# Performance work log

Hardware: AMD Instinct MI355X
Metric: run time of the kernel (lower is better)

Reference implementation:

```python
import jax, jax.numpy as jnp
import numpy as np

B, S, D, H = 2, 2048, 768, 12
DK = D // H
NEG = -1000000000.0


def setup_inputs() -> dict:
    key = jax.random.key(0)
    ks = jax.random.split(key, 12)
    inp = {
        "query": jax.random.normal(ks[0], (B, S, D), jnp.float32),
        "key": jax.random.normal(ks[1], (B, S, D), jnp.float32),
        "value": jax.random.normal(ks[2], (B, S, D), jnp.float32),
        "mask": jax.random.randint(ks[3], (B, 1, 1, S), 0, 2, jnp.int32),
    }
    sc = 1.0 / np.sqrt(D)
    inp["Wq"] = jax.random.normal(ks[4], (D, D), jnp.float32) * sc
    inp["bq"] = jnp.zeros((D,), jnp.float32)
    inp["Wk"] = jax.random.normal(ks[5], (D, D), jnp.float32) * sc
    inp["bk"] = jnp.zeros((D,), jnp.float32)
    inp["Wv"] = jax.random.normal(ks[6], (D, D), jnp.float32) * sc
    inp["bv"] = jnp.zeros((D,), jnp.float32)
    inp["Wo"] = jax.random.normal(ks[7], (D, D), jnp.float32) * sc
    inp["bo"] = jnp.zeros((D,), jnp.float32)
    return inp


def reference(query, key, value, mask, Wq, bq, Wk, bk, Wv, bv, Wo, bo):
    b = query.shape[0]
    # QKV projections -> [B, H, S, DK]
    def proj(x, W, bias):
        y = jnp.einsum('bsd,de->bse', x, W.T) + bias
        return y.reshape(b, -1, H, DK).transpose(0, 2, 1, 3)
    q = proj(query, Wq, bq)
    k = proj(key, Wk, bk)
    v = proj(value, Wv, bv)
    # scores: [B, H, S, S]
    scores = jnp.einsum('bhqd,bhkd->bhqk', q, k) / jnp.sqrt(jnp.float32(DK))
    scores = jnp.where(mask == 0, jnp.float32(NEG), scores)
    p = jax.nn.softmax(scores, axis=-1)
    x = jnp.einsum('bhqk,bhkd->bhqd', p, v)  # [B, H, S, DK]
    x = x.transpose(0, 2, 1, 3).reshape(b, -1, H * DK)
    return jnp.einsum('bsd,de->bse', x, Wo.T) + bo
```

## Files before the change

### kernel.cpp

```cpp
#include <hip/hip_runtime.h>

typedef unsigned short u16;
typedef __attribute__((ext_vector_type(8))) __bf16 bf16x8;
typedef __attribute__((ext_vector_type(8))) short s16x8;
typedef __attribute__((ext_vector_type(8))) unsigned short u16x8;
typedef __attribute__((ext_vector_type(4))) float f32x4;
typedef __attribute__((ext_vector_type(4))) unsigned short u16x4;
typedef __attribute__((ext_vector_type(4))) float fl4;
typedef __attribute__((ext_vector_type(4))) int i32x4;

#define MFMA(a, b, c) __builtin_amdgcn_mfma_f32_16x16x32_bf16((a), (b), (c), 0, 0, 0)
#define QSC 0.18033688011112042f

__device__ __forceinline__ u16 f2bf(float f) {
  union { float f; unsigned u; } v; v.f = f;
  unsigned u = v.u;
  return (u16)((u + 0x7fffu + ((u >> 16) & 1u)) >> 16);
}

__device__ __forceinline__ float bf2f(u16 u) {
  union { unsigned u; float f; } v; v.u = ((unsigned)u) << 16;
  return v.f;
}

__device__ __forceinline__ void gll16(const u16* g, u16* l) {
  typedef __attribute__((address_space(1))) unsigned int gu32;
  typedef __attribute__((address_space(3))) unsigned int lu32;
  __builtin_amdgcn_global_load_lds((gu32*)g, (lu32*)l, 16, 0, 0);
}


__global__ __launch_bounds__(256) void k_convert_x(
    const float* __restrict__ q, const float* __restrict__ k,
    const float* __restrict__ v, u16* __restrict__ xb) {
  const int NG = 4096 * 768 / 4;
  const int n = 3 * NG;
  for (int i = blockIdx.x * 256 + threadIdx.x; i < n; i += gridDim.x * 256) {
    int seg = i / NG;
    int j = (i - seg * NG) * 4;
    const float* s = (seg == 0) ? q : ((seg == 1) ? k : v);
    fl4 f = *(const fl4*)(s + j);
    u16x4 o;
    o[0] = f2bf(f[0]); o[1] = f2bf(f[1]); o[2] = f2bf(f[2]); o[3] = f2bf(f[3]);
    *(u16x4*)(xb + seg * (4096 * 768) + j) = o;
  }
}

__global__ __launch_bounds__(256) void k_convert_w(
    const float* __restrict__ Wq, const float* __restrict__ Wk,
    const float* __restrict__ Wv, const float* __restrict__ Wo,
    u16* __restrict__ wqkv, u16* __restrict__ wob) {
  const int n = 3072 * 192;
  for (int i = blockIdx.x * 256 + threadIdx.x; i < n; i += gridDim.x * 256) {
    int row = i / 192;
    int col = (i - row * 192) * 4;
    const float* src; u16* dst; float sc = 1.0f;
    if (row < 768)       { src = Wq + row * 768;          dst = wqkv + row * 768; sc = QSC; }
    else if (row < 1536) { src = Wk + (row - 768) * 768;  dst = wqkv + row * 768; }
    else if (row < 2304) { src = Wv + (row - 1536) * 768; dst = wqkv + row * 768; }
    else                 { src = Wo + (row - 2304) * 768; dst = wob + (row - 2304) * 768; }
    fl4 f = *(const fl4*)(src + col);
    u16x4 o;
    o[0] = f2bf(f[0] * sc); o[1] = f2bf(f[1] * sc);
    o[2] = f2bf(f[2] * sc); o[3] = f2bf(f[3] * sc);
    *(u16x4*)(dst + col) = o;
  }
}


__global__ __launch_bounds__(256) void k_gemm_qkv(
    const u16* __restrict__ xb, const u16* __restrict__ wqkv,
    const float* __restrict__ bq, const float* __restrict__ bk_,
    const float* __restrict__ bv_,
    u16* __restrict__ Qb, u16* __restrict__ Kb, u16* __restrict__ Vtb) {
  __shared__ __align__(16) u16 As[128 * 32];
  __shared__ __align__(16) u16 Bs[128 * 32];
  const int tid = threadIdx.x;
  const int row0 = blockIdx.x * 128, col0 = blockIdx.y * 128;
  const int seg = col0 / 768;
  const u16* A = xb + (size_t)seg * (4096 * 768);
  const int w = tid >> 6, lane = tid & 63, lr = lane & 15, kg = lane >> 4;
  const int wr = (w >> 1) * 64, wc = (w & 1) * 64;

  const int c0 = tid, c1 = tid + 256;
  const int r0c = c0 >> 2, p0 = c0 & 3, g0 = p0 ^ ((r0c >> 1) & 3);
  const int r1c = c1 >> 2, p1 = c1 & 3, g1 = p1 ^ ((r1c >> 1) & 3);

  f32x4 acc[4][4];
  f32x4 zero = {0.f, 0.f, 0.f, 0.f};
#pragma unroll
  for (int i = 0; i < 4; i++)
#pragma unroll
    for (int j = 0; j < 4; j++) acc[i][j] = zero;

  int aoff[4], boff[4];
#pragma unroll
  for (int mi = 0; mi < 4; mi++) {
    int r = wr + mi * 16 + lr;
    aoff[mi] = r * 32 + (kg ^ ((r >> 1) & 3)) * 8;
  }
#pragma unroll
  for (int ni = 0; ni < 4; ni++) {
    int r = wc + ni * 16 + lr;
    boff[ni] = r * 32 + (kg ^ ((r >> 1) & 3)) * 8;
  }

  for (int kt = 0; kt < 24; kt++) {
    const int k0 = kt * 32;
    gll16(A + (row0 + r0c) * 768 + k0 + g0 * 8, As + c0 * 8);
    gll16(A + (row0 + r1c) * 768 + k0 + g1 * 8, As + c1 * 8);
    gll16(wqkv + (col0 + r0c) * 768 + k0 + g0 * 8, Bs + c0 * 8);
    gll16(wqkv + (col0 + r1c) * 768 + k0 + g1 * 8, Bs + c1 * 8);
    __syncthreads();
    bf16x8 af[4], bfr[4];
#pragma unroll
    for (int mi = 0; mi < 4; mi++) af[mi] = *(const bf16x8*)(As + aoff[mi]);
#pragma unroll
    for (int ni = 0; ni < 4; ni++) bfr[ni] = *(const bf16x8*)(Bs + boff[ni]);
#pragma unroll
    for (int mi = 0; mi < 4; mi++)
#pragma unroll
      for (int ni = 0; ni < 4; ni++)
        acc[mi][ni] = MFMA(af[mi], bfr[ni], acc[mi][ni]);
    __syncthreads();
  }

  const float* bias = (seg == 0) ? bq : ((seg == 1) ? bk_ : bv_);
  const float bsc = (seg == 0) ? QSC : 1.0f;
  const int ncol0 = col0 - seg * 768;
#pragma unroll
  for (int ni = 0; ni < 4; ni++) {
    const int n = ncol0 + wc + ni * 16 + lr;
    const float bval = bias[n] * bsc;
    const int hh = n >> 6, dk = n & 63;
#pragma unroll
    for (int mi = 0; mi < 4; mi++)
#pragma unroll
      for (int j = 0; j < 4; j++) {
        const int m = row0 + wr + mi * 16 + kg * 4 + j;
        const int bb = m >> 11, ss = m & 2047;
        const u16 val = f2bf(acc[mi][ni][j] + bval);
        if (seg == 0)
          Qb[((size_t)((bb * 12 + hh) * 2048 + ss)) * 64 + dk] = val;
        else if (seg == 1)
          Kb[((size_t)((bb * 12 + hh) * 2048 + ss)) * 64 + dk] = val;
        else
          Vtb[((size_t)((bb * 12 + hh) * 64 + dk)) * 2048 + ss] = val;
      }
  }
}


__global__ __launch_bounds__(256) void k_attn(
    const u16* __restrict__ Qb, const u16* __restrict__ Kb,
    const u16* __restrict__ Vtb, const int* __restrict__ mask,
    u16* __restrict__ o_part, float* __restrict__ l_part) {
  __shared__ __align__(16) u16 Ks[2][64 * 64];
  __shared__ __align__(16) u16 Vs[2][64 * 64];
  __shared__ __align__(16) u16 Ps[4][32 * 64];
  __shared__ __align__(16) int mlds[1024];
  const int bh = blockIdx.y, b = bh / 12;
  const int half = blockIdx.z;
  const int kvb = half << 10;
  const int tid = threadIdx.x, w = tid >> 6, lane = tid & 63;
  const int lr = lane & 15, g = lane >> 4;
  const int q0 = blockIdx.x * 128 + w * 32;
  const u16* Qh = Qb + (size_t)bh * (2048 * 64);
  const u16* Kh = Kb + (size_t)bh * (2048 * 64);
  const u16* Vh = Vtb + (size_t)bh * (64 * 2048);
  const int* mb = mask + b * 2048;
  u16* Pw = Ps[w];

  *(i32x4*)(mlds + tid * 4) = *(const i32x4*)(mb + kvb + tid * 4);

  bf16x8 aq[2][2];
#pragma unroll
  for (int mi = 0; mi < 2; mi++)
#pragma unroll
    for (int ks = 0; ks < 2; ks++)
      aq[mi][ks] = *(const bf16x8*)(Qh + (q0 + mi * 16 + lr) * 64 + ks * 32 + g * 8);

  f32x4 zero = {0.f, 0.f, 0.f, 0.f};
  f32x4 o[2][4];
#pragma unroll
  for (int mi = 0; mi < 2; mi++)
#pragma unroll
    for (int di = 0; di < 4; di++) o[mi][di] = zero;
  f32x4 o_l[2];
  o_l[0] = zero; o_l[1] = zero;

  s16x8 ov = {0x3F80, 0x3F80, 0x3F80, 0x3F80, 0x3F80, 0x3F80, 0x3F80, 0x3F80};
  bf16x8 ones = __builtin_bit_cast(bf16x8, ov);

  const int c0 = tid, c1 = tid + 256;
  const int sr0 = c0 >> 3, sg0 = (c0 & 7) ^ (sr0 & 7);
  const int sr1 = c1 >> 3, sg1 = (c1 & 7) ^ (sr1 & 7);
  const u16* kA0 = Kh + (size_t)kvb * 64 + sr0 * 64 + sg0 * 8;
  const u16* kA1 = Kh + (size_t)kvb * 64 + sr1 * 64 + sg1 * 8;
  const u16* vA0 = Vh + sr0 * 2048 + kvb + sg0 * 8;
  const u16* vA1 = Vh + sr1 * 2048 + kvb + sg1 * 8;

#define STAGE(u) { u16* kd = Ks[(u)&1]; u16* vd = Vs[(u)&1];           \
    gll16(kA0 + (u) * 4096, kd + c0 * 8);                              \
    gll16(kA1 + (u) * 4096, kd + c1 * 8);                              \
    gll16(vA0 + (u) * 64,  vd + c0 * 8);                               \
    gll16(vA1 + (u) * 64,  vd + c1 * 8); }

  STAGE(0);
  __syncthreads();

  for (int t = 0; t < 16; t++) {
    if (t < 15) STAGE(t + 1);
    const u16* Kc = Ks[t & 1];
    const u16* Vc = Vs[t & 1];

    f32x4 s[2][4];
#pragma unroll
    for (int ni = 0; ni < 4; ni++) {
      const int row = ni * 16 + lr;
      bf16x8 b0 = *(const bf16x8*)(Kc + row * 64 + ((g ^ (row & 7)) << 3));
      bf16x8 b1 = *(const bf16x8*)(Kc + row * 64 + (((4 + g) ^ (row & 7)) << 3));
#pragma unroll
      for (int mi = 0; mi < 2; mi++) {
        f32x4 z = zero;
        z = MFMA(aq[mi][0], b0, z);
        z = MFMA(aq[mi][1], b1, z);
        s[mi][ni] = z;
      }
    }
    int mk[4];
#pragma unroll
    for (int ni = 0; ni < 4; ni++) mk[ni] = mlds[t * 64 + ni * 16 + lr];
#pragma unroll
    for (int mi = 0; mi < 2; mi++)
#pragma unroll
      for (int ni = 0; ni < 4; ni++)
#pragma unroll
        for (int j = 0; j < 4; j++)
          s[mi][ni][j] = mk[ni] ? s[mi][ni][j] : -1e9f;

#pragma unroll
    for (int mi = 0; mi < 2; mi++)
#pragma unroll
      for (int ni = 0; ni < 4; ni++)
#pragma unroll
        for (int j = 0; j < 4; j++) {
          const float p = __builtin_amdgcn_exp2f(s[mi][ni][j]);
          const int prow = mi * 16 + g * 4 + j;
          const int byt = prow * 128 + ((ni * 32 + lr * 2) ^ ((prow & 7) << 4));
          Pw[byt >> 1] = f2bf(p);
        }

#pragma unroll
    for (int ks2 = 0; ks2 < 2; ks2++) {
      bf16x8 ap[2];
#pragma unroll
      for (int mi = 0; mi < 2; mi++) {
        const int prow = mi * 16 + lr;
        const int byt = prow * 128 + ((ks2 * 64 + g * 16) ^ ((prow & 7) << 4));
        ap[mi] = *(const bf16x8*)(Pw + (byt >> 1));
      }
#pragma unroll
      for (int di = 0; di < 4; di++) {
        const int vrow = di * 16 + lr;
        bf16x8 bv = *(const bf16x8*)(Vc + vrow * 64 + (((ks2 * 4 + g) ^ (vrow & 7)) << 3));
#pragma unroll
        for (int mi = 0; mi < 2; mi++)
          o[mi][di] = MFMA(ap[mi], bv, o[mi][di]);
      }
#pragma unroll
      for (int mi = 0; mi < 2; mi++)
        o_l[mi] = MFMA(ap[mi], ones, o_l[mi]);
    }

    if (t < 15) __syncthreads();
  }
#undef STAGE

  u16* opw = o_part + (size_t)(half * 24 + bh) * (2048 * 64);
  float* lpw = l_part + (size_t)(half * 24 + bh) * 2048;
#pragma unroll
  for (int mi = 0; mi < 2; mi++) {
#pragma unroll
    for (int di = 0; di < 4; di++)
#pragma unroll
      for (int j = 0; j < 4; j++) {
        const int row = q0 + mi * 16 + g * 4 + j;
        opw[(size_t)row * 64 + di * 16 + lr] = f2bf(o[mi][di][j]);
      }
    if (lr == 0) {
#pragma unroll
      for (int j = 0; j < 4; j++)
        lpw[q0 + mi * 16 + g * 4 + j] = o_l[mi][j];
    }
  }
}


__global__ __launch_bounds__(256) void k_combine(
    const u16* __restrict__ o_part, const float* __restrict__ l_part,
    u16* __restrict__ attn) {
  const int idx = blockIdx.x * 256 + threadIdx.x;
  const int row = idx >> 3;
  const int c8 = (idx & 7) << 3;
  const size_t HALF_O = (size_t)24 * 2048 * 64;
  u16x8 a0 = *(const u16x8*)(o_part + (size_t)row * 64 + c8);
  u16x8 a1 = *(const u16x8*)(o_part + HALF_O + (size_t)row * 64 + c8);
  const float l = l_part[row] + l_part[24 * 2048 + row];
  const float rcp = 1.0f / l;
  u16x8 r;
#pragma unroll
  for (int j = 0; j < 8; j++)
    r[j] = f2bf((bf2f(a0[j]) + bf2f(a1[j])) * rcp);
  const int bh = row >> 11, s = row & 2047;
  const int b = bh / 12, h = bh - b * 12;
  *(u16x8*)(attn + (size_t)(b * 2048 + s) * 768 + h * 64 + c8) = r;
}


__global__ __launch_bounds__(256) void k_gemm_out(
    const u16* __restrict__ attn, const u16* __restrict__ wob,
    const float* __restrict__ bo, float* __restrict__ out) {
  __shared__ __align__(16) u16 As[128 * 32];
  __shared__ __align__(16) u16 Bs[128 * 32];
  const int tid = threadIdx.x;
  const int row0 = blockIdx.x * 128, col0 = blockIdx.y * 128;
  const int w = tid >> 6, lane = tid & 63, lr = lane & 15, kg = lane >> 4;
  const int wr = (w >> 1) * 64, wc = (w & 1) * 64;

  const int c0 = tid, c1 = tid + 256;
  const int r0c = c0 >> 2, p0 = c0 & 3, g0 = p0 ^ ((r0c >> 1) & 3);
  const int r1c = c1 >> 2, p1 = c1 & 3, g1 = p1 ^ ((r1c >> 1) & 3);

  f32x4 acc[4][4];
  f32x4 zero = {0.f, 0.f, 0.f, 0.f};
#pragma unroll
  for (int i = 0; i < 4; i++)
#pragma unroll
    for (int j = 0; j < 4; j++) acc[i][j] = zero;

  int aoff[4], boff[4];
#pragma unroll
  for (int mi = 0; mi < 4; mi++) {
    int r = wr + mi * 16 + lr;
    aoff[mi] = r * 32 + (kg ^ ((r >> 1) & 3)) * 8;
  }
#pragma unroll
  for (int ni = 0; ni < 4; ni++) {
    int r = wc + ni * 16 + lr;
    boff[ni] = r * 32 + (kg ^ ((r >> 1) & 3)) * 8;
  }

  for (int kt = 0; kt < 24; kt++) {
    const int k0 = kt * 32;
    gll16(attn + (row0 + r0c) * 768 + k0 + g0 * 8, As + c0 * 8);
    gll16(attn + (row0 + r1c) * 768 + k0 + g1 * 8, As + c1 * 8);
    gll16(wob + (col0 + r0c) * 768 + k0 + g0 * 8, Bs + c0 * 8);
    gll16(wob + (col0 + r1c) * 768 + k0 + g1 * 8, Bs + c1 * 8);
    __syncthreads();
    bf16x8 af[4], bfr[4];
#pragma unroll
    for (int mi = 0; mi < 4; mi++) af[mi] = *(const bf16x8*)(As + aoff[mi]);
#pragma unroll
    for (int ni = 0; ni < 4; ni++) bfr[ni] = *(const bf16x8*)(Bs + boff[ni]);
#pragma unroll
    for (int mi = 0; mi < 4; mi++)
#pragma unroll
      for (int ni = 0; ni < 4; ni++)
        acc[mi][ni] = MFMA(af[mi], bfr[ni], acc[mi][ni]);
    __syncthreads();
  }

#pragma unroll
  for (int ni = 0; ni < 4; ni++) {
    const int n = col0 + wc + ni * 16 + lr;
    const float bval = bo[n];
#pragma unroll
    for (int mi = 0; mi < 4; mi++)
#pragma unroll
      for (int j = 0; j < 4; j++) {
        const int m = row0 + wr + mi * 16 + kg * 4 + j;
        out[(size_t)m * 768 + n] = acc[mi][ni][j] + bval;
      }
  }
}


extern "C" void kernel_launch(void* const* d_in, const int* in_sizes, int n_in,
                              void* d_out, int out_size, void* d_ws, size_t ws_size,
                              hipStream_t stream) {
  const float* q = (const float*)d_in[0];
  const float* k = (const float*)d_in[1];
  const float* v = (const float*)d_in[2];
  const int* mask = (const int*)d_in[3];
  const float* Wq = (const float*)d_in[4];
  const float* bq = (const float*)d_in[5];
  const float* Wk = (const float*)d_in[6];
  const float* bk = (const float*)d_in[7];
  const float* Wv = (const float*)d_in[8];
  const float* bv = (const float*)d_in[9];
  const float* Wo = (const float*)d_in[10];
  const float* bo = (const float*)d_in[11];
  float* out = (float*)d_out;

  u16* xb = (u16*)d_ws;
  u16* wqkv = xb + (size_t)3 * 4096 * 768;
  u16* wob = wqkv + (size_t)2304 * 768;
  u16* Qb = wob + (size_t)768 * 768;
  u16* Kb = Qb + (size_t)4096 * 768;
  u16* Vtb = Kb + (size_t)4096 * 768;
  u16* attn = Vtb + (size_t)4096 * 768;

  u16* o_part = xb;
  float* l_part = (float*)(xb + (size_t)2 * 24 * 2048 * 64);

  k_convert_x<<<dim3(4608), dim3(256), 0, stream>>>(q, k, v, xb);
  k_convert_w<<<dim3(2304), dim3(256), 0, stream>>>(Wq, Wk, Wv, Wo, wqkv, wob);
  k_gemm_qkv<<<dim3(32, 18), dim3(256), 0, stream>>>(xb, wqkv, bq, bk, bv, Qb, Kb, Vtb);
  k_attn<<<dim3(16, 24, 2), dim3(256), 0, stream>>>(Qb, Kb, Vtb, mask, o_part, l_part);
  k_combine<<<dim3(1536), dim3(256), 0, stream>>>(o_part, l_part, attn);
  k_gemm_out<<<dim3(32, 6), dim3(256), 0, stream>>>(attn, wob, bo, out);
}
```

Measured before the change: 123.7 us.

## Fuse fp32-to-bf16 input conversion into QKV GEMM and double-buffer GEMM tiles

Removes the separate activation conversion kernel: the QKV GEMM now loads fp32 inputs into registers, converts them to bf16 and writes them to LDS. Both GEMMs gain double-buffered LDS tiles so the next k-tile's loads are issued before the current tile's MFMAs. The f2bf helper switches to the compiler's native bf16 cast. This trades one kernel launch and a round trip of 3x4096x768 bf16 data for heavier register traffic in the QKV GEMM, with each A tile now read as fp32 once per column-block, roughly six times per segment.

```diff
diff --git a/kernel.cpp b/kernel.cpp
--- a/kernel.cpp
+++ b/kernel.cpp
@@ -13,9 +13,8 @@
 #define QSC 0.18033688011112042f
 
 __device__ __forceinline__ u16 f2bf(float f) {
-  union { float f; unsigned u; } v; v.f = f;
-  unsigned u = v.u;
-  return (u16)((u + 0x7fffu + ((u >> 16) & 1u)) >> 16);
+  __bf16 h = (__bf16)f;
+  return __builtin_bit_cast(unsigned short, h);
 }
 
 __device__ __forceinline__ float bf2f(u16 u) {
@@ -29,22 +28,6 @@
   __builtin_amdgcn_global_load_lds((gu32*)g, (lu32*)l, 16, 0, 0);
 }
 
-
-__global__ __launch_bounds__(256) void k_convert_x(
-    const float* __restrict__ q, const float* __restrict__ k,
-    const float* __restrict__ v, u16* __restrict__ xb) {
-  const int NG = 4096 * 768 / 4;
-  const int n = 3 * NG;
-  for (int i = blockIdx.x * 256 + threadIdx.x; i < n; i += gridDim.x * 256) {
-    int seg = i / NG;
-    int j = (i - seg * NG) * 4;
-    const float* s = (seg == 0) ? q : ((seg == 1) ? k : v);
-    fl4 f = *(const fl4*)(s + j);
-    u16x4 o;
-    o[0] = f2bf(f[0]); o[1] = f2bf(f[1]); o[2] = f2bf(f[2]); o[3] = f2bf(f[3]);
-    *(u16x4*)(xb + seg * (4096 * 768) + j) = o;
-  }
-}
 
 __global__ __launch_bounds__(256) void k_convert_w(
     const float* __restrict__ Wq, const float* __restrict__ Wk,
@@ -69,22 +52,27 @@
 
 
 __global__ __launch_bounds__(256) void k_gemm_qkv(
-    const u16* __restrict__ xb, const u16* __restrict__ wqkv,
+    const float* __restrict__ xq, const float* __restrict__ xk,
+    const float* __restrict__ xv, const u16* __restrict__ wqkv,
     const float* __restrict__ bq, const float* __restrict__ bk_,
     const float* __restrict__ bv_,
     u16* __restrict__ Qb, u16* __restrict__ Kb, u16* __restrict__ Vtb) {
-  __shared__ __align__(16) u16 As[128 * 32];
-  __shared__ __align__(16) u16 Bs[128 * 32];
+  __shared__ __align__(16) u16 Abuf[2][128 * 32];
+  __shared__ __align__(16) u16 Bbuf[2][128 * 32];
   const int tid = threadIdx.x;
   const int row0 = blockIdx.x * 128, col0 = blockIdx.y * 128;
   const int seg = col0 / 768;
-  const u16* A = xb + (size_t)seg * (4096 * 768);
+  const float* A32 = (seg == 0) ? xq : ((seg == 1) ? xk : xv);
   const int w = tid >> 6, lane = tid & 63, lr = lane & 15, kg = lane >> 4;
   const int wr = (w >> 1) * 64, wc = (w & 1) * 64;
 
   const int c0 = tid, c1 = tid + 256;
   const int r0c = c0 >> 2, p0 = c0 & 3, g0 = p0 ^ ((r0c >> 1) & 3);
   const int r1c = c1 >> 2, p1 = c1 & 3, g1 = p1 ^ ((r1c >> 1) & 3);
+  const float* aS0 = A32 + (size_t)(row0 + r0c) * 768 + g0 * 8;
+  const float* aS1 = A32 + (size_t)(row0 + r1c) * 768 + g1 * 8;
+  const u16* bS0 = wqkv + (size_t)(col0 + r0c) * 768 + g0 * 8;
+  const u16* bS1 = wqkv + (size_t)(col0 + r1c) * 768 + g1 * 8;
 
   f32x4 acc[4][4];
   f32x4 zero = {0.f, 0.f, 0.f, 0.f};
@@ -105,25 +93,47 @@
     boff[ni] = r * 32 + (kg ^ ((r >> 1) & 3)) * 8;
   }
 
+  fl4 ar[4];
+#define LOADA(kt) { ar[0] = *(const fl4*)(aS0 + (kt) * 32);       \
+                    ar[1] = *(const fl4*)(aS0 + (kt) * 32 + 4);   \
+                    ar[2] = *(const fl4*)(aS1 + (kt) * 32);       \
+                    ar[3] = *(const fl4*)(aS1 + (kt) * 32 + 4); }
+#define WRITEA(buf) { u16x8 t0, t1;                               \
+    t0[0]=f2bf(ar[0][0]); t0[1]=f2bf(ar[0][1]); t0[2]=f2bf(ar[0][2]); t0[3]=f2bf(ar[0][3]); \
+    t0[4]=f2bf(ar[1][0]); t0[5]=f2bf(ar[1][1]); t0[6]=f2bf(ar[1][2]); t0[7]=f2bf(ar[1][3]); \
+    t1[0]=f2bf(ar[2][0]); t1[1]=f2bf(ar[2][1]); t1[2]=f2bf(ar[2][2]); t1[3]=f2bf(ar[2][3]); \
+    t1[4]=f2bf(ar[3][0]); t1[5]=f2bf(ar[3][1]); t1[6]=f2bf(ar[3][2]); t1[7]=f2bf(ar[3][3]); \
+    *(u16x8*)((buf) + c0 * 8) = t0; *(u16x8*)((buf) + c1 * 8) = t1; }
+#define STAGEB(kt, buf) { gll16(bS0 + (kt) * 32, (buf) + c0 * 8); \
+                          gll16(bS1 + (kt) * 32, (buf) + c1 * 8); }
+
+  LOADA(0);
+  STAGEB(0, Bbuf[0]);
+  WRITEA(Abuf[0]);
+  __syncthreads();
+
   for (int kt = 0; kt < 24; kt++) {
-    const int k0 = kt * 32;
-    gll16(A + (row0 + r0c) * 768 + k0 + g0 * 8, As + c0 * 8);
-    gll16(A + (row0 + r1c) * 768 + k0 + g1 * 8, As + c1 * 8);
-    gll16(wqkv + (col0 + r0c) * 768 + k0 + g0 * 8, Bs + c0 * 8);
-    gll16(wqkv + (col0 + r1c) * 768 + k0 + g1 * 8, Bs + c1 * 8);
-    __syncthreads();
+    const int cur = kt & 1;
+    if (kt < 23) { LOADA(kt + 1); STAGEB(kt + 1, Bbuf[cur ^ 1]); }
     bf16x8 af[4], bfr[4];
 #pragma unroll
-    for (int mi = 0; mi < 4; mi++) af[mi] = *(const bf16x8*)(As + aoff[mi]);
-#pragma unroll
-    for (int ni = 0; ni < 4; ni++) bfr[ni] = *(const bf16x8*)(Bs + boff[ni]);
+    for (int mi = 0; mi < 4; mi++) af[mi] = *(const bf16x8*)(Abuf[cur] + aoff[mi]);
+#pragma unroll
+    for (int ni = 0; ni < 4; ni++) bfr[ni] = *(const bf16x8*)(Bbuf[cur] + boff[ni]);
 #pragma unroll
     for (int mi = 0; mi < 4; mi++)
 #pragma unroll
       for (int ni = 0; ni < 4; ni++)
         acc[mi][ni] = MFMA(af[mi], bfr[ni], acc[mi][ni]);
     __syncthreads();
-  }
+    if (kt < 23) {
+      WRITEA(Abuf[cur ^ 1]);
+      __syncthreads();
+    }
+  }
+#undef LOADA
+#undef WRITEA
+#undef STAGEB
 
   const float* bias = (seg == 0) ? bq : ((seg == 1) ? bk_ : bv_);
   const float bsc = (seg == 0) ? QSC : 1.0f;
@@ -321,8 +331,8 @@
 __global__ __launch_bounds__(256) void k_gemm_out(
     const u16* __restrict__ attn, const u16* __restrict__ wob,
     const float* __restrict__ bo, float* __restrict__ out) {
-  __shared__ __align__(16) u16 As[128 * 32];
-  __shared__ __align__(16) u16 Bs[128 * 32];
+  __shared__ __align__(16) u16 As[2][128 * 32];
+  __shared__ __align__(16) u16 Bs[2][128 * 32];
   const int tid = threadIdx.x;
   const int row0 = blockIdx.x * 128, col0 = blockIdx.y * 128;
   const int w = tid >> 6, lane = tid & 63, lr = lane & 15, kg = lane >> 4;
@@ -331,6 +341,10 @@
   const int c0 = tid, c1 = tid + 256;
   const int r0c = c0 >> 2, p0 = c0 & 3, g0 = p0 ^ ((r0c >> 1) & 3);
   const int r1c = c1 >> 2, p1 = c1 & 3, g1 = p1 ^ ((r1c >> 1) & 3);
+  const u16* aS0 = attn + (size_t)(row0 + r0c) * 768 + g0 * 8;
+  const u16* aS1 = attn + (size_t)(row0 + r1c) * 768 + g1 * 8;
+  const u16* bS0 = wob + (size_t)(col0 + r0c) * 768 + g0 * 8;
+  const u16* bS1 = wob + (size_t)(col0 + r1c) * 768 + g1 * 8;
 
   f32x4 acc[4][4];
   f32x4 zero = {0.f, 0.f, 0.f, 0.f};
@@ -351,25 +365,31 @@
     boff[ni] = r * 32 + (kg ^ ((r >> 1) & 3)) * 8;
   }
 
+#define STAGE(kt) { u16* ad = As[(kt)&1]; u16* bd = Bs[(kt)&1];   \
+    gll16(aS0 + (kt) * 32, ad + c0 * 8);                          \
+    gll16(aS1 + (kt) * 32, ad + c1 * 8);                          \
+    gll16(bS0 + (kt) * 32, bd + c0 * 8);                          \
+    gll16(bS1 + (kt) * 32, bd + c1 * 8); }
+
+  STAGE(0);
+  __syncthreads();
+
   for (int kt = 0; kt < 24; kt++) {
-    const int k0 = kt * 32;
-    gll16(attn + (row0 + r0c) * 768 + k0 + g0 * 8, As + c0 * 8);
-    gll16(attn + (row0 + r1c) * 768 + k0 + g1 * 8, As + c1 * 8);
-    gll16(wob + (col0 + r0c) * 768 + k0 + g0 * 8, Bs + c0 * 8);
-    gll16(wob + (col0 + r1c) * 768 + k0 + g1 * 8, Bs + c1 * 8);
-    __syncthreads();
+    const int cur = kt & 1;
+    if (kt < 23) STAGE(kt + 1);
     bf16x8 af[4], bfr[4];
 #pragma unroll
-    for (int mi = 0; mi < 4; mi++) af[mi] = *(const bf16x8*)(As + aoff[mi]);
-#pragma unroll
-    for (int ni = 0; ni < 4; ni++) bfr[ni] = *(const bf16x8*)(Bs + boff[ni]);
+    for (int mi = 0; mi < 4; mi++) af[mi] = *(const bf16x8*)(As[cur] + aoff[mi]);
+#pragma unroll
+    for (int ni = 0; ni < 4; ni++) bfr[ni] = *(const bf16x8*)(Bs[cur] + boff[ni]);
 #pragma unroll
     for (int mi = 0; mi < 4; mi++)
 #pragma unroll
       for (int ni = 0; ni < 4; ni++)
         acc[mi][ni] = MFMA(af[mi], bfr[ni], acc[mi][ni]);
-    __syncthreads();
-  }
+    if (kt < 23) __syncthreads();
+  }
+#undef STAGE
 
 #pragma unroll
   for (int ni = 0; ni < 4; ni++) {
@@ -403,20 +423,19 @@
   const float* bo = (const float*)d_in[11];
   float* out = (float*)d_out;
 
-  u16* xb = (u16*)d_ws;
-  u16* wqkv = xb + (size_t)3 * 4096 * 768;
+  u16* scratch = (u16*)d_ws;
+  u16* wqkv = scratch + (size_t)3 * 4096 * 768;
   u16* wob = wqkv + (size_t)2304 * 768;
   u16* Qb = wob + (size_t)768 * 768;
   u16* Kb = Qb + (size_t)4096 * 768;
   u16* Vtb = Kb + (size_t)4096 * 768;
   u16* attn = Vtb + (size_t)4096 * 768;
 
-  u16* o_part = xb;
-  float* l_part = (float*)(xb + (size_t)2 * 24 * 2048 * 64);
-
-  k_convert_x<<<dim3(4608), dim3(256), 0, stream>>>(q, k, v, xb);
+  u16* o_part = scratch;
+  float* l_part = (float*)(scratch + (size_t)2 * 24 * 2048 * 64);
+
   k_convert_w<<<dim3(2304), dim3(256), 0, stream>>>(Wq, Wk, Wv, Wo, wqkv, wob);
-  k_gemm_qkv<<<dim3(32, 18), dim3(256), 0, stream>>>(xb, wqkv, bq, bk, bv, Qb, Kb, Vtb);
+  k_gemm_qkv<<<dim3(32, 18), dim3(256), 0, stream>>>(q, k, v, wqkv, bq, bk, bv, Qb, Kb, Vtb);
   k_attn<<<dim3(16, 24, 2), dim3(256), 0, stream>>>(Qb, Kb, Vtb, mask, o_part, l_part);
   k_combine<<<dim3(1536), dim3(256), 0, stream>>>(o_part, l_part, attn);
   k_gemm_out<<<dim3(32, 6), dim3(256), 0, stream>>>(attn, wob, bo, out);
```

Measured after the change: 123.6 us. No clear change (-0.1%).
